# Kernel tuning notes

Hardware: AMD Instinct MI355X
Metric: run time of the kernel (lower is better)

Reference implementation:

```python
import jax, jax.numpy as jnp
import numpy as np

N_NODES = 100000
N_EDGES = 1600000
D_NODE = 96
D_EDGE = 32
N_GRAPHS = 128
BN_EPS = 1e-5


def setup_inputs() -> dict:
    key = jax.random.key(0)
    ks = jax.random.split(key, 8)
    x = jax.random.normal(ks[0], (N_NODES, D_NODE), dtype=jnp.float32)
    edge_attr = jax.random.normal(ks[1], (N_EDGES, D_EDGE), dtype=jnp.float32)
    edge_index = jax.random.randint(ks[2], (2, N_EDGES), 0, N_NODES, dtype=jnp.int64)
    batch = jnp.sort(jax.random.randint(ks[3], (N_NODES,), 0, N_GRAPHS, dtype=jnp.int64))
    W1 = jax.random.normal(ks[4], (16, D_NODE + D_EDGE), dtype=jnp.float32) * 0.09
    b1 = jax.random.normal(ks[5], (16,), dtype=jnp.float32) * 0.01
    gamma = jnp.ones((16,), dtype=jnp.float32)
    beta = jnp.zeros((16,), dtype=jnp.float32)
    run_mean = jnp.zeros((16,), dtype=jnp.float32)
    run_var = jnp.ones((16,), dtype=jnp.float32)
    W2 = jax.random.normal(ks[6], (1, 16), dtype=jnp.float32) * 0.25
    b2 = jax.random.normal(ks[7], (1,), dtype=jnp.float32) * 0.01
    return {"x": x, "edge_attr": edge_attr, "edge_index": edge_index, "batch": batch,
            "W1": W1, "b1": b1, "gamma": gamma, "beta": beta,
            "run_mean": run_mean, "run_var": run_var, "W2": W2, "b2": b2}


def reference(x, edge_attr, edge_index, batch, W1, b1, gamma, beta, run_mean, run_var, W2, b2):
    src, dst = edge_index[0], edge_index[1]
    # per-edge message: MLP(cat([x_j, edge_attr]))  -- [E, d_node+d_edge]
    msg_in = jnp.concatenate([x[src], edge_attr], axis=1)
    h = msg_in @ W1.T + b1                                  # [E, 16]
    # BatchNorm1d in eval mode (running stats); Dropout is identity in eval
    h = gamma * (h - run_mean) * jax.lax.rsqrt(run_var + BN_EPS) + beta
    h = jax.nn.relu(h)
    msg = h @ W2.T + b2                                     # [E, 1]
    # scatter-add messages to target nodes
    node_out = jax.ops.segment_sum(msg, dst, num_segments=N_NODES)   # [N, 1]
    # global add pool per graph
    pooled = jax.ops.segment_sum(node_out, batch, num_segments=N_GRAPHS)  # [G, 1]
    # mean over feature dim (size 1)
    return jnp.mean(pooled, axis=1)                         # [G]
```

## Files before the change

### kernel.cpp

```cpp
#include <hip/hip_runtime.h>

#define N_NODES 100000
#define N_EDGES 1600000
#define D_NODE 96
#define D_EDGE 32
#define N_GRAPHS 128
#define BN_EPS 1e-5f

#define EDGE_BLOCKS 6250
#define EDGE_THREADS 256

typedef float f2 __attribute__((ext_vector_type(2)));

__global__ void prep_kernel(const float* __restrict__ W1, const float* __restrict__ b1,
                            const float* __restrict__ gamma, const float* __restrict__ beta,
                            const float* __restrict__ rmean, const float* __restrict__ rvar,
                            const float* __restrict__ W2, const float* __restrict__ b2,
                            float* __restrict__ w1nT, float* __restrict__ w1eT,
                            float* __restrict__ cw) {
    int t = threadIdx.x;
    if (t < 16) {
        float A = gamma[t] * rsqrtf(rvar[t] + BN_EPS);
        cw[t] = A * (b1[t] - rmean[t]) + beta[t];
        cw[16 + t] = W2[t];
        for (int j = 0; j < D_NODE; ++j)
            w1nT[j * 16 + t] = A * W1[t * (D_NODE + D_EDGE) + j];
        for (int j = 0; j < D_EDGE; ++j)
            w1eT[j * 16 + t] = A * W1[t * (D_NODE + D_EDGE) + D_NODE + j];
    }
    if (t == 16) cw[32] = b2[0];
}

__global__ __launch_bounds__(256) void node_proj_kernel(const float* __restrict__ x,
                                                        const float* __restrict__ w1nT,
                                                        float* __restrict__ y) {
    int t = threadIdx.x;
    int q = t >> 6;
    int n = blockIdx.x * 64 + (t & 63);
    if (n >= N_NODES) return;
    const float4* xr = (const float4*)(x + (size_t)n * D_NODE);
    f2 acc0 = {0.f, 0.f}, acc1 = {0.f, 0.f};
#pragma unroll
    for (int j4 = 0; j4 < D_NODE / 4; ++j4) {
        float4 xv = xr[j4];
#pragma unroll
        for (int u = 0; u < 4; ++u) {
            float xs = (u == 0) ? xv.x : (u == 1) ? xv.y : (u == 2) ? xv.z : xv.w;
            f2 xs2 = {xs, xs};
            const f2* wp = (const f2*)(w1nT + (j4 * 4 + u) * 16 + q * 4);
            acc0 = __builtin_elementwise_fma(xs2, wp[0], acc0);
            acc1 = __builtin_elementwise_fma(xs2, wp[1], acc1);
        }
    }
    ((float4*)(y + (size_t)n * 16))[q] = make_float4(acc0.x, acc0.y, acc1.x, acc1.y);
}

__global__ __launch_bounds__(EDGE_THREADS, 8) void edge_kernel(
    const float* __restrict__ ea, const int* __restrict__ eidx,
    const int* __restrict__ batch, const float* __restrict__ y,
    const float* __restrict__ w1eT, const float* __restrict__ cw,
    float* __restrict__ partials) {
    __shared__ float bins[N_GRAPHS];
    int t = threadIdx.x;
    if (t < N_GRAPHS) bins[t] = 0.f;
    __syncthreads();

    int e = blockIdx.x * EDGE_THREADS + t;

    int sn = eidx[e];
    int dn = eidx[N_EDGES + e];
    int g  = batch[dn];

    float ya[16];
    const float4* yr = (const float4*)(y + (size_t)sn * 16);
#pragma unroll
    for (int qq = 0; qq < 4; ++qq) ((float4*)ya)[qq] = yr[qq];

    const float4* er = (const float4*)(ea + (size_t)e * D_EDGE);
    float4 ev[8];
#pragma unroll
    for (int i = 0; i < 8; ++i) ev[i] = er[i];

    f2 acc[8];
#pragma unroll
    for (int k2 = 0; k2 < 8; ++k2) acc[k2] = (f2){0.f, 0.f};

    const float* evs = (const float*)ev;
#pragma unroll
    for (int j = 0; j < D_EDGE; ++j) {
        float b = evs[j];
        f2 b2 = {b, b};
        const f2* wp = (const f2*)(w1eT + j * 16);
#pragma unroll
        for (int k2 = 0; k2 < 8; ++k2)
            acc[k2] = __builtin_elementwise_fma(b2, wp[k2], acc[k2]);
    }

    const f2* ya2 = (const f2*)ya;
    const f2* c2  = (const f2*)cw;
    const f2* w2p = (const f2*)(cw + 16);
    f2 m2 = {0.f, 0.f};
#pragma unroll
    for (int k2 = 0; k2 < 8; ++k2) {
        f2 h = acc[k2] + ya2[k2] + c2[k2];
        h = __builtin_elementwise_max(h, (f2){0.f, 0.f});
        m2 = __builtin_elementwise_fma(h, w2p[k2], m2);
    }
    float msg = m2.x + m2.y + cw[32];

    atomicAdd(&bins[g], msg);

    __syncthreads();
    if (t < N_GRAPHS) partials[(size_t)blockIdx.x * N_GRAPHS + t] = bins[t];
}

__global__ __launch_bounds__(256) void reduce_kernel(const float* __restrict__ partials,
                                                     float* __restrict__ out) {
    __shared__ float sm[256];
    int g = blockIdx.x;
    float acc = 0.f;
    for (int b = threadIdx.x; b < EDGE_BLOCKS; b += 256)
        acc += partials[(size_t)b * N_GRAPHS + g];
    sm[threadIdx.x] = acc;
    __syncthreads();
    for (int w = 128; w > 0; w >>= 1) {
        if (threadIdx.x < w) sm[threadIdx.x] += sm[threadIdx.x + w];
        __syncthreads();
    }
    if (threadIdx.x == 0) out[g] = sm[0];
}

extern "C" void kernel_launch(void* const* d_in, const int* in_sizes, int n_in,
                              void* d_out, int out_size, void* d_ws, size_t ws_size,
                              hipStream_t stream) {
    const float* x     = (const float*)d_in[0];
    const float* ea    = (const float*)d_in[1];
    const int*   eidx  = (const int*)d_in[2];
    const int*   batch = (const int*)d_in[3];
    const float* W1    = (const float*)d_in[4];
    const float* b1    = (const float*)d_in[5];
    const float* gamma = (const float*)d_in[6];
    const float* beta  = (const float*)d_in[7];
    const float* rmean = (const float*)d_in[8];
    const float* rvar  = (const float*)d_in[9];
    const float* W2    = (const float*)d_in[10];
    const float* b2    = (const float*)d_in[11];
    float* out = (float*)d_out;

    float* ws = (float*)d_ws;
    float* w1nT     = ws;
    float* w1eT     = ws + 1536;
    float* cw       = ws + 2048;
    float* y        = ws + 4096;
    float* partials = ws + 4096 + (size_t)N_NODES * 16;

    prep_kernel<<<1, 64, 0, stream>>>(W1, b1, gamma, beta, rmean, rvar, W2, b2, w1nT, w1eT, cw);
    node_proj_kernel<<<(N_NODES + 63) / 64, 256, 0, stream>>>(x, w1nT, y);
    edge_kernel<<<EDGE_BLOCKS, EDGE_THREADS, 0, stream>>>(ea, eidx, batch, y, w1eT, cw, partials);
    reduce_kernel<<<N_GRAPHS, 256, 0, stream>>>(partials, out);
}
```

Measured before the change: 413.8 us.

## Double-buffer edge attributes into LDS via async global_load_lds across chunks

```diff
diff --git a/kernel.cpp b/kernel.cpp
--- a/kernel.cpp
+++ b/kernel.cpp
@@ -1,4 +1,5 @@
 #include <hip/hip_runtime.h>
+#include <stdint.h>
 
 #define N_NODES 100000
 #define N_EDGES 1600000
@@ -7,10 +8,18 @@
 #define N_GRAPHS 128
 #define BN_EPS 1e-5f
 
-#define EDGE_BLOCKS 6250
-#define EDGE_THREADS 256
+#define EB_THREADS 256
+#define CHUNK 256
+#define CHUNKS_PER_BLOCK 5
+#define EB_BLOCKS 1250
 
 typedef float f2 __attribute__((ext_vector_type(2)));
+
+__device__ __forceinline__ void stage16(const float* g, float* l) {
+    __builtin_amdgcn_global_load_lds(
+        (const __attribute__((address_space(1))) void*)g,
+        (__attribute__((address_space(3))) void*)l, 16, 0, 0);
+}
 
 __global__ void prep_kernel(const float* __restrict__ W1, const float* __restrict__ b1,
                             const float* __restrict__ gamma, const float* __restrict__ beta,
@@ -34,12 +43,12 @@
 __global__ __launch_bounds__(256) void node_proj_kernel(const float* __restrict__ x,
                                                         const float* __restrict__ w1nT,
                                                         float* __restrict__ y) {
-    int t = threadIdx.x;
-    int q = t >> 6;
-    int n = blockIdx.x * 64 + (t & 63);
+    int n = blockIdx.x * 256 + threadIdx.x;
     if (n >= N_NODES) return;
     const float4* xr = (const float4*)(x + (size_t)n * D_NODE);
-    f2 acc0 = {0.f, 0.f}, acc1 = {0.f, 0.f};
+    f2 acc[8];
+#pragma unroll
+    for (int k2 = 0; k2 < 8; ++k2) acc[k2] = (f2){0.f, 0.f};
 #pragma unroll
     for (int j4 = 0; j4 < D_NODE / 4; ++j4) {
         float4 xv = xr[j4];
@@ -47,70 +56,108 @@
         for (int u = 0; u < 4; ++u) {
             float xs = (u == 0) ? xv.x : (u == 1) ? xv.y : (u == 2) ? xv.z : xv.w;
             f2 xs2 = {xs, xs};
-            const f2* wp = (const f2*)(w1nT + (j4 * 4 + u) * 16 + q * 4);
-            acc0 = __builtin_elementwise_fma(xs2, wp[0], acc0);
-            acc1 = __builtin_elementwise_fma(xs2, wp[1], acc1);
-        }
-    }
-    ((float4*)(y + (size_t)n * 16))[q] = make_float4(acc0.x, acc0.y, acc1.x, acc1.y);
-}
-
-__global__ __launch_bounds__(EDGE_THREADS, 8) void edge_kernel(
+            const f2* wp = (const f2*)(w1nT + (j4 * 4 + u) * 16);
+#pragma unroll
+            for (int k2 = 0; k2 < 8; ++k2)
+                acc[k2] = __builtin_elementwise_fma(xs2, wp[k2], acc[k2]);
+        }
+    }
+    float4* yr = (float4*)(y + (size_t)n * 16);
+#pragma unroll
+    for (int q = 0; q < 4; ++q)
+        yr[q] = make_float4(acc[2 * q].x, acc[2 * q].y, acc[2 * q + 1].x, acc[2 * q + 1].y);
+}
+
+__global__ __launch_bounds__(EB_THREADS, 2) void edge_kernel(
     const float* __restrict__ ea, const int* __restrict__ eidx,
     const int* __restrict__ batch, const float* __restrict__ y,
     const float* __restrict__ w1eT, const float* __restrict__ cw,
     float* __restrict__ partials) {
+    __shared__ float4 ebuf[2][CHUNK * 8];
     __shared__ float bins[N_GRAPHS];
-    int t = threadIdx.x;
+    const int t = threadIdx.x;
     if (t < N_GRAPHS) bins[t] = 0.f;
+
+    const int wave = t >> 6;
+    const int g8 = (t & 63) >> 3;
+    const int s8 = t & 7;
+    const int f4log = s8 ^ g8;
+
+    const int base = blockIdx.x * (CHUNKS_PER_BLOCK * CHUNK);
+
+    {
+        const float* sb = ea + (size_t)base * D_EDGE;
+#pragma unroll
+        for (int i = 0; i < 8; ++i) {
+            int k = wave * 8 + i;
+            int e = k * 8 + g8;
+            stage16(sb + (size_t)e * D_EDGE + f4log * 4, (float*)&ebuf[0][k * 64]);
+        }
+    }
+    asm volatile("s_waitcnt vmcnt(0)" ::: "memory");
     __syncthreads();
 
-    int e = blockIdx.x * EDGE_THREADS + t;
-
-    int sn = eidx[e];
-    int dn = eidx[N_EDGES + e];
-    int g  = batch[dn];
-
-    float ya[16];
-    const float4* yr = (const float4*)(y + (size_t)sn * 16);
-#pragma unroll
-    for (int qq = 0; qq < 4; ++qq) ((float4*)ya)[qq] = yr[qq];
-
-    const float4* er = (const float4*)(ea + (size_t)e * D_EDGE);
-    float4 ev[8];
-#pragma unroll
-    for (int i = 0; i < 8; ++i) ev[i] = er[i];
-
-    f2 acc[8];
-#pragma unroll
-    for (int k2 = 0; k2 < 8; ++k2) acc[k2] = (f2){0.f, 0.f};
-
-    const float* evs = (const float*)ev;
-#pragma unroll
-    for (int j = 0; j < D_EDGE; ++j) {
-        float b = evs[j];
-        f2 b2 = {b, b};
-        const f2* wp = (const f2*)(w1eT + j * 16);
-#pragma unroll
-        for (int k2 = 0; k2 < 8; ++k2)
-            acc[k2] = __builtin_elementwise_fma(b2, wp[k2], acc[k2]);
-    }
-
-    const f2* ya2 = (const f2*)ya;
-    const f2* c2  = (const f2*)cw;
-    const f2* w2p = (const f2*)(cw + 16);
-    f2 m2 = {0.f, 0.f};
-#pragma unroll
-    for (int k2 = 0; k2 < 8; ++k2) {
-        f2 h = acc[k2] + ya2[k2] + c2[k2];
-        h = __builtin_elementwise_max(h, (f2){0.f, 0.f});
-        m2 = __builtin_elementwise_fma(h, w2p[k2], m2);
-    }
-    float msg = m2.x + m2.y + cw[32];
-
-    atomicAdd(&bins[g], msg);
-
-    __syncthreads();
+    float b2v = cw[32];
+    int cur = 0;
+#pragma unroll 1
+    for (int c = 0; c < CHUNKS_PER_BLOCK; ++c) {
+        int cb = base + c * CHUNK;
+
+        if (c + 1 < CHUNKS_PER_BLOCK) {
+            const float* sb = ea + (size_t)(cb + CHUNK) * D_EDGE;
+#pragma unroll
+            for (int i = 0; i < 8; ++i) {
+                int k = wave * 8 + i;
+                int e = k * 8 + g8;
+                stage16(sb + (size_t)e * D_EDGE + f4log * 4, (float*)&ebuf[cur ^ 1][k * 64]);
+            }
+        }
+
+        int e = cb + t;
+        int sn = eidx[e];
+        int dn = eidx[N_EDGES + e];
+        int g = batch[dn];
+
+        float ya[16];
+        const float4* yr = (const float4*)(y + (size_t)sn * 16);
+#pragma unroll
+        for (int qq = 0; qq < 4; ++qq) ((float4*)ya)[qq] = yr[qq];
+
+        float4 ev[8];
+#pragma unroll
+        for (int f = 0; f < 8; ++f) ev[f] = ebuf[cur][t * 8 + (f ^ (t & 7))];
+
+        f2 acc[8];
+#pragma unroll
+        for (int k2 = 0; k2 < 8; ++k2) acc[k2] = (f2){0.f, 0.f};
+        const float* evs = (const float*)ev;
+#pragma unroll
+        for (int j = 0; j < D_EDGE; ++j) {
+            float b = evs[j];
+            f2 bb = {b, b};
+            const f2* wp = (const f2*)(w1eT + j * 16);
+#pragma unroll
+            for (int k2 = 0; k2 < 8; ++k2)
+                acc[k2] = __builtin_elementwise_fma(bb, wp[k2], acc[k2]);
+        }
+
+        const f2* ya2 = (const f2*)ya;
+        const f2* c2 = (const f2*)cw;
+        const f2* w2p = (const f2*)(cw + 16);
+        f2 m2 = {0.f, 0.f};
+#pragma unroll
+        for (int k2 = 0; k2 < 8; ++k2) {
+            f2 h = acc[k2] + ya2[k2] + c2[k2];
+            h = __builtin_elementwise_max(h, (f2){0.f, 0.f});
+            m2 = __builtin_elementwise_fma(h, w2p[k2], m2);
+        }
+        atomicAdd(&bins[g], m2.x + m2.y + b2v);
+
+        asm volatile("s_waitcnt vmcnt(0)" ::: "memory");
+        __syncthreads();
+        cur ^= 1;
+    }
+
     if (t < N_GRAPHS) partials[(size_t)blockIdx.x * N_GRAPHS + t] = bins[t];
 }
 
@@ -119,7 +166,7 @@
     __shared__ float sm[256];
     int g = blockIdx.x;
     float acc = 0.f;
-    for (int b = threadIdx.x; b < EDGE_BLOCKS; b += 256)
+    for (int b = threadIdx.x; b < EB_BLOCKS; b += 256)
         acc += partials[(size_t)b * N_GRAPHS + g];
     sm[threadIdx.x] = acc;
     __syncthreads();
@@ -155,7 +202,7 @@
     float* partials = ws + 4096 + (size_t)N_NODES * 16;
 
     prep_kernel<<<1, 64, 0, stream>>>(W1, b1, gamma, beta, rmean, rvar, W2, b2, w1nT, w1eT, cw);
-    node_proj_kernel<<<(N_NODES + 63) / 64, 256, 0, stream>>>(x, w1nT, y);
-    edge_kernel<<<EDGE_BLOCKS, EDGE_THREADS, 0, stream>>>(ea, eidx, batch, y, w1eT, cw, partials);
+    node_proj_kernel<<<(N_NODES + 255) / 256, 256, 0, stream>>>(x, w1nT, y);
+    edge_kernel<<<EB_BLOCKS, EB_THREADS, 0, stream>>>(ea, eidx, batch, y, w1eT, cw, partials);
     reduce_kernel<<<N_GRAPHS, 256, 0, stream>>>(partials, out);
 }
```

Measured after the change: 374.4 us. 9.5% less time.
